# Optimization experiments

Measured on AMD Instinct MI355X. Metric: run time of the kernel, lower is better.

## Reference

```python
import jax, jax.numpy as jnp
import numpy as np

B, H, E, L = 2048, 4096, 8, 512
TAU = 1.0


def setup_inputs() -> dict:
    key = jax.random.key(0)
    k1, k2, k3, k4 = jax.random.split(key, 4)
    hidden = jax.random.normal(k1, (B, H), dtype=jnp.float32)
    envs = jax.random.normal(k2, (B, E), dtype=jnp.float32)
    idx = jnp.arange(B, dtype=jnp.int64)
    gumbel = jax.random.gumbel(k3, (B, E), dtype=jnp.float32)
    W = jax.random.normal(k4, (E, L, H), dtype=jnp.float32) * (1.0 / np.sqrt(H))
    return {"hidden": hidden, "envs": envs, "idx": idx, "gumbel": gumbel, "W": W}


def _hard_gumbel_softmax(log_probs, gumbel, tau):
    # F.gumbel_softmax(log_probs, tau=1, hard=True) with pre-sampled gumbel noise
    y_soft = jax.nn.softmax((log_probs + gumbel) / tau, axis=-1)
    y_hard = jax.nn.one_hot(jnp.argmax(y_soft, axis=-1), y_soft.shape[-1], dtype=y_soft.dtype)
    # straight-through estimator
    return y_hard + y_soft - jax.lax.stop_gradient(y_soft)


def reference(hidden, envs, idx, gumbel, W):
    # gating: env = gumbel_softmax(log_softmax(envs[idx]))  -> [B, E]
    log_probs = jax.nn.log_softmax(envs[idx], axis=-1)
    env = _hard_gumbel_softmax(log_probs, gumbel, TAU)
    # per-expert logits: [B, E, L]; fuses the per-sample python loop
    expert_logits = jnp.einsum("bh,elh->bel", hidden, W)
    # gating combine: [B, L]
    logits = jnp.einsum("be,bel->bl", env, expert_logits)
    # variance penalty over expert weights
    W_mean = jnp.mean(W, axis=0)  # [L, H]
    diff_sq = jnp.sum((W - W_mean[None]) ** 2, axis=(1, 2))  # ||W_e - W_mean||_2^2 per expert
    l1 = jnp.sum(jnp.abs(W), axis=(1, 2))                    # ||W_e||_1 per expert
    loss_penalty = jnp.mean(diff_sq / (l1 ** 2))
    return logits, loss_penalty
```

## Files before the change

### kernel.cpp

```cpp
#include <hip/hip_runtime.h>
#include <hip/hip_bf16.h>

constexpr int B = 2048, H = 4096, E = 8, L = 512;
constexpr int LH = L * H;

typedef float f4v __attribute__((ext_vector_type(4)));
typedef short short8 __attribute__((ext_vector_type(8)));

constexpr int BT = 128;
constexpr int LT = 128;
constexpr int KT = 32;
constexpr int SK = 4;
constexpr int RTMAX = 3;
constexpr int NITER = (H / SK) / KT;

constexpr int NGEMM = E * 4 * 4 * RTMAX;
constexpr int NPEN = 2048;

constexpr size_t WS_COUNTS = 0;
constexpr size_t WS_ACCUM = 32;
constexpr size_t WS_ROWLIST = 128;

using as1_u32 = const __attribute__((address_space(1))) unsigned int;
using as3_u32 = __attribute__((address_space(3))) unsigned int;

static __device__ __forceinline__ void dma16(const float* g, float* lds) {
  __builtin_amdgcn_global_load_lds((as1_u32*)g, (as3_u32*)lds, 16, 0, 0);
}

static __device__ __forceinline__ unsigned pk2(float a, float b) {
  __hip_bfloat162 p = __float22bfloat162_rn(make_float2(a, b));
  unsigned u;
  __builtin_memcpy(&u, &p, 4);
  return u;
}

static __device__ __forceinline__ short8 cvt8(f4v lo, f4v hi) {
  union { short8 s; unsigned u[4]; } r;
  r.u[0] = pk2(lo.x, lo.y);
  r.u[1] = pk2(lo.z, lo.w);
  r.u[2] = pk2(hi.x, hi.y);
  r.u[3] = pk2(hi.z, hi.w);
  return r.s;
}

__global__ void prep_kernel(const float* __restrict__ envs,
                            const float* __restrict__ gumbel,
                            int* __restrict__ counts,
                            float* __restrict__ accum,
                            int* __restrict__ row_list,
                            float* __restrict__ out) {
  const int t = threadIdx.x;
  const int id = blockIdx.x;
  if (id < E) {
    __shared__ int lcnt;
    if (t == 0) lcnt = 0;
    if (id == 0) {
      if (t < 16) accum[t] = 0.f;
    }
    __syncthreads();
#pragma unroll
    for (int r = 0; r < 8; ++r) {
      int b = r * 256 + t;
      f4v e0 = *(const f4v*)(envs + b * E);
      f4v e1 = *(const f4v*)(envs + b * E + 4);
      f4v g0 = *(const f4v*)(gumbel + b * E);
      f4v g1 = *(const f4v*)(gumbel + b * E + 4);
      float z[8] = {e0.x + g0.x, e0.y + g0.y, e0.z + g0.z, e0.w + g0.w,
                    e1.x + g1.x, e1.y + g1.y, e1.z + g1.z, e1.w + g1.w};
      float zmax = z[0];
      int am = 0;
#pragma unroll
      for (int e = 1; e < E; ++e)
        if (z[e] > zmax) { zmax = z[e]; am = e; }
      if (am == id) {
        int pos = atomicAdd(&lcnt, 1);
        row_list[id * B + pos] = b;
      }
    }
    __syncthreads();
    if (t == 0) counts[id] = lcnt;
  } else {
    const int cb = id - E;
    f4v z = {0.f, 0.f, 0.f, 0.f};
    f4v* dst = (f4v*)out + (size_t)cb * 1024;
#pragma unroll
    for (int i = 0; i < 4; ++i) dst[i * 256 + t] = z;
  }
}

__launch_bounds__(256, 2)
__global__ void fused_kernel(const float* __restrict__ hidden,
                             const float* __restrict__ W,
                             const int* __restrict__ counts,
                             const int* __restrict__ row_list,
                             float* __restrict__ out,
                             float* __restrict__ accum) {
  const int id = blockIdx.x;
  const int t = threadIdx.x;

  __shared__ __align__(16) float AshF[2][BT * KT];
  __shared__ __align__(16) float BshF[2][LT * KT];
  __shared__ int rlsh[BT];
  __shared__ float red[4][16];

  if (id >= NGEMM) {
    const int p = (id - NGEMM) * 256 + t;

    f4v w[E];
    float mx = 0.f, my = 0.f, mz = 0.f, mw = 0.f;
#pragma unroll
    for (int e = 0; e < E; ++e) {
      w[e] = __builtin_nontemporal_load(
          (const f4v*)(W + (size_t)e * LH + (size_t)p * 4));
      mx += w[e].x; my += w[e].y; mz += w[e].z; mw += w[e].w;
    }
    mx *= 0.125f; my *= 0.125f; mz *= 0.125f; mw *= 0.125f;

    float vals[16];
#pragma unroll
    for (int e = 0; e < E; ++e) {
      float dx = w[e].x - mx, dy = w[e].y - my, dz = w[e].z - mz,
            dw = w[e].w - mw;
      vals[e] = dx * dx + dy * dy + dz * dz + dw * dw;
      vals[8 + e] =
          fabsf(w[e].x) + fabsf(w[e].y) + fabsf(w[e].z) + fabsf(w[e].w);
    }
#pragma unroll
    for (int k = 0; k < 16; ++k) {
      float v = vals[k];
      for (int off = 32; off > 0; off >>= 1) v += __shfl_xor(v, off);
      vals[k] = v;
    }
    const int wv = t >> 6, lane = t & 63;
    if (lane == 0) {
#pragma unroll
      for (int k = 0; k < 16; ++k) red[wv][k] = vals[k];
    }
    __syncthreads();
    if (t < 16) {
      atomicAdd(&accum[t], red[0][t] + red[1][t] + red[2][t] + red[3][t]);
    }
    return;
  }

  const int e = id & 7;
  const int lt = (id >> 3) & 3;
  const int sk = (id >> 5) & 3;
  const int rt = id >> 7;

  const int cnt = counts[e];
  const int rbase = rt * BT;
  if (rbase >= cnt) return;
  const int lbase = lt * LT;

  if (t < BT) {
    int rr = rbase + t;
    rlsh[t] = row_list[e * B + (rr < cnt ? rr : (cnt - 1))];
  }
  __syncthreads();

  const float* Wp = W + (size_t)e * LH + (size_t)lbase * H;

  const int wave = t >> 6;
  const int lane = t & 63;
  const int quad = lane >> 4;
  const int l16 = lane & 15;
  const int wm = (wave >> 1) * 64;
  const int wn = (wave & 1) * 64;

  const int kbeg = sk * (H / SK);
  const int srow = lane >> 3;
  const int sblk = lane & 7;

  const float* sp[8];
  float* sl[2][8];
  const bool stageA = (wave < 2);
#pragma unroll
  for (int i = 0; i < 8; ++i) {
    int r = (stageA ? wave : (wave - 2)) * 64 + i * 8 + srow;
    int gblk = sblk ^ (r & 7);
    if (stageA) {
      sp[i] = hidden + (size_t)rlsh[r] * H + kbeg + gblk * 4;
      sl[0][i] = &AshF[0][(r - srow) * KT];
      sl[1][i] = &AshF[1][(r - srow) * KT];
    } else {
      sp[i] = Wp + (size_t)r * H + kbeg + gblk * 4;
      sl[0][i] = &BshF[0][(r - srow) * KT];
      sl[1][i] = &BshF[1][(r - srow) * KT];
    }
  }

  auto stage = [&](int buf) {
#pragma unroll
    for (int i = 0; i < 8; ++i) {
      dma16(sp[i], sl[buf][i]);
      sp[i] += KT;
    }
  };

  const int r7 = l16 & 7;
  const int slo = (2 * quad) ^ r7;
  const int shi = slo ^ 1;

  f4v acc[4][4] = {};

  stage(0);

  for (int it = 0; it < NITER; ++it) {
    const int buf = it & 1;
    __syncthreads();
    if (it + 1 < NITER) stage(buf ^ 1);

    short8 af[4], bf[4];
#pragma unroll
    for (int i = 0; i < 4; ++i) {
      int ra = wm + i * 16 + l16;
      f4v lo = *(const f4v*)&AshF[buf][ra * KT + slo * 4];
      f4v hi = *(const f4v*)&AshF[buf][ra * KT + shi * 4];
      af[i] = cvt8(lo, hi);
    }
#pragma unroll
    for (int j = 0; j < 4; ++j) {
      int rb = wn + j * 16 + l16;
      f4v lo = *(const f4v*)&BshF[buf][rb * KT + slo * 4];
      f4v hi = *(const f4v*)&BshF[buf][rb * KT + shi * 4];
      bf[j] = cvt8(lo, hi);
    }
#pragma unroll
    for (int i = 0; i < 4; ++i)
#pragma unroll
      for (int j = 0; j < 4; ++j)
        acc[i][j] =
            __builtin_amdgcn_mfma_f32_16x16x32_bf16(af[i], bf[j], acc[i][j],
                                                    0, 0, 0);
  }

#pragma unroll
  for (int i = 0; i < 4; ++i) {
#pragma unroll
    for (int j = 0; j < 4; ++j) {
#pragma unroll
      for (int reg = 0; reg < 4; ++reg) {
        int rloc = wm + i * 16 + quad * 4 + reg;
        if (rbase + rloc < cnt) {
          int bidx = rlsh[rloc];
          atomicAdd(&out[(size_t)bidx * L + lbase + wn + j * 16 + l16],
                    acc[i][j][reg]);
        }
      }
    }
  }
}

__global__ void finalize_kernel(const float* __restrict__ accum,
                                float* __restrict__ out) {
  if (threadIdx.x == 0) {
    float loss = 0.f;
#pragma unroll
    for (int e = 0; e < E; ++e) {
      float l1 = accum[8 + e];
      loss += accum[e] / (l1 * l1);
    }
    out[(size_t)B * L] = loss * 0.125f;
  }
}

extern "C" void kernel_launch(void* const* d_in, const int* in_sizes, int n_in,
                              void* d_out, int out_size, void* d_ws,
                              size_t ws_size, hipStream_t stream) {
  (void)in_sizes; (void)n_in; (void)ws_size; (void)out_size;
  const float* hidden = (const float*)d_in[0];
  const float* envs   = (const float*)d_in[1];
  const float* gumbel = (const float*)d_in[3];
  const float* W      = (const float*)d_in[4];
  float* out = (float*)d_out;

  char* ws = (char*)d_ws;
  int*   counts   = (int*)(ws + WS_COUNTS);
  float* accum    = (float*)(ws + WS_ACCUM);
  int*   row_list = (int*)(ws + WS_ROWLIST);

  prep_kernel<<<dim3(E + 256), dim3(256), 0, stream>>>(envs, gumbel, counts,
                                                       accum, row_list, out);
  fused_kernel<<<dim3(NGEMM + NPEN), dim3(256), 0, stream>>>(
      hidden, W, counts, row_list, out, accum);
  finalize_kernel<<<dim3(1), dim3(64), 0, stream>>>(accum, out);
}
```

Measured before the change: 173.2 us.

## Convert tiles to bf16 in registers before LDS and fold finalize into penalty blocks

```diff
diff --git a/kernel.cpp b/kernel.cpp
--- a/kernel.cpp
+++ b/kernel.cpp
@@ -10,6 +10,7 @@
 constexpr int BT = 128;
 constexpr int LT = 128;
 constexpr int KT = 32;
+constexpr int LROW = KT + 8;
 constexpr int SK = 4;
 constexpr int RTMAX = 3;
 constexpr int NITER = (H / SK) / KT;
@@ -19,14 +20,8 @@
 
 constexpr size_t WS_COUNTS = 0;
 constexpr size_t WS_ACCUM = 32;
+constexpr size_t WS_DONE = 96;
 constexpr size_t WS_ROWLIST = 128;
-
-using as1_u32 = const __attribute__((address_space(1))) unsigned int;
-using as3_u32 = __attribute__((address_space(3))) unsigned int;
-
-static __device__ __forceinline__ void dma16(const float* g, float* lds) {
-  __builtin_amdgcn_global_load_lds((as1_u32*)g, (as3_u32*)lds, 16, 0, 0);
-}
 
 static __device__ __forceinline__ unsigned pk2(float a, float b) {
   __hip_bfloat162 p = __float22bfloat162_rn(make_float2(a, b));
@@ -35,19 +30,24 @@
   return u;
 }
 
-static __device__ __forceinline__ short8 cvt8(f4v lo, f4v hi) {
-  union { short8 s; unsigned u[4]; } r;
-  r.u[0] = pk2(lo.x, lo.y);
-  r.u[1] = pk2(lo.z, lo.w);
-  r.u[2] = pk2(hi.x, hi.y);
-  r.u[3] = pk2(hi.z, hi.w);
-  return r.s;
+static __device__ __forceinline__ uint2 cvt4(f4v v) {
+  uint2 r;
+  r.x = pk2(v.x, v.y);
+  r.y = pk2(v.z, v.w);
+  return r;
+}
+
+static __device__ __forceinline__ void tbar() {
+  asm volatile("s_waitcnt lgkmcnt(0)" ::: "memory");
+  __builtin_amdgcn_s_barrier();
+  asm volatile("" ::: "memory");
 }
 
 __global__ void prep_kernel(const float* __restrict__ envs,
                             const float* __restrict__ gumbel,
                             int* __restrict__ counts,
                             float* __restrict__ accum,
+                            int* __restrict__ done,
                             int* __restrict__ row_list,
                             float* __restrict__ out) {
   const int t = threadIdx.x;
@@ -57,6 +57,7 @@
     if (t == 0) lcnt = 0;
     if (id == 0) {
       if (t < 16) accum[t] = 0.f;
+      if (t == 16) *done = 0;
     }
     __syncthreads();
 #pragma unroll
@@ -89,18 +90,19 @@
   }
 }
 
-__launch_bounds__(256, 2)
+__launch_bounds__(256, 3)
 __global__ void fused_kernel(const float* __restrict__ hidden,
                              const float* __restrict__ W,
                              const int* __restrict__ counts,
                              const int* __restrict__ row_list,
                              float* __restrict__ out,
-                             float* __restrict__ accum) {
+                             float* __restrict__ accum,
+                             int* __restrict__ done) {
   const int id = blockIdx.x;
   const int t = threadIdx.x;
 
-  __shared__ __align__(16) float AshF[2][BT * KT];
-  __shared__ __align__(16) float BshF[2][LT * KT];
+  __shared__ __align__(16) short Ash[2][BT * LROW];
+  __shared__ __align__(16) short Bsh[2][LT * LROW];
   __shared__ int rlsh[BT];
   __shared__ float red[4][16];
 
@@ -141,6 +143,21 @@
     if (t < 16) {
       atomicAdd(&accum[t], red[0][t] + red[1][t] + red[2][t] + red[3][t]);
     }
+    asm volatile("s_waitcnt vmcnt(0)" ::: "memory");
+    if (t == 0) {
+      int prev = __hip_atomic_fetch_add(done, 1, __ATOMIC_RELAXED,
+                                        __HIP_MEMORY_SCOPE_AGENT);
+      if (prev == NPEN - 1) {
+        float loss = 0.f;
+#pragma unroll
+        for (int e = 0; e < E; ++e) {
+          float d = atomicAdd(&accum[e], 0.f);
+          float l1 = atomicAdd(&accum[8 + e], 0.f);
+          loss += d / (l1 * l1);
+        }
+        out[(size_t)B * L] = loss * 0.125f;
+      }
+    }
     return;
   }
 
@@ -174,59 +191,55 @@
   const int sblk = lane & 7;
 
   const float* sp[8];
-  float* sl[2][8];
+  short* sw[8];
   const bool stageA = (wave < 2);
 #pragma unroll
   for (int i = 0; i < 8; ++i) {
     int r = (stageA ? wave : (wave - 2)) * 64 + i * 8 + srow;
-    int gblk = sblk ^ (r & 7);
     if (stageA) {
-      sp[i] = hidden + (size_t)rlsh[r] * H + kbeg + gblk * 4;
-      sl[0][i] = &AshF[0][(r - srow) * KT];
-      sl[1][i] = &AshF[1][(r - srow) * KT];
+      sp[i] = hidden + (size_t)rlsh[r] * H + kbeg + sblk * 4;
+      sw[i] = &Ash[0][r * LROW + sblk * 4];
     } else {
-      sp[i] = Wp + (size_t)r * H + kbeg + gblk * 4;
-      sl[0][i] = &BshF[0][(r - srow) * KT];
-      sl[1][i] = &BshF[1][(r - srow) * KT];
-    }
-  }
-
-  auto stage = [&](int buf) {
+      sp[i] = Wp + (size_t)r * H + kbeg + sblk * 4;
+      sw[i] = &Bsh[0][r * LROW + sblk * 4];
+    }
+  }
+
+  f4v g[8];
+  auto load8 = [&]() {
 #pragma unroll
     for (int i = 0; i < 8; ++i) {
-      dma16(sp[i], sl[buf][i]);
+      g[i] = *(const f4v*)sp[i];
       sp[i] += KT;
     }
   };
-
-  const int r7 = l16 & 7;
-  const int slo = (2 * quad) ^ r7;
-  const int shi = slo ^ 1;
+  auto write8 = [&](int buf) {
+#pragma unroll
+    for (int i = 0; i < 8; ++i) {
+      uint2 p = cvt4(g[i]);
+      *(uint2*)(sw[i] + buf * (BT * LROW)) = p;
+    }
+  };
 
   f4v acc[4][4] = {};
 
-  stage(0);
+  load8();
 
   for (int it = 0; it < NITER; ++it) {
     const int buf = it & 1;
-    __syncthreads();
-    if (it + 1 < NITER) stage(buf ^ 1);
-
+    write8(buf);
+    tbar();
+    if (it + 1 < NITER) load8();
+
+    const short* As = &Ash[0][0] + buf * (BT * LROW);
+    const short* Bs = &Bsh[0][0] + buf * (BT * LROW);
     short8 af[4], bf[4];
 #pragma unroll
-    for (int i = 0; i < 4; ++i) {
-      int ra = wm + i * 16 + l16;
-      f4v lo = *(const f4v*)&AshF[buf][ra * KT + slo * 4];
-      f4v hi = *(const f4v*)&AshF[buf][ra * KT + shi * 4];
-      af[i] = cvt8(lo, hi);
-    }
-#pragma unroll
-    for (int j = 0; j < 4; ++j) {
-      int rb = wn + j * 16 + l16;
-      f4v lo = *(const f4v*)&BshF[buf][rb * KT + slo * 4];
-      f4v hi = *(const f4v*)&BshF[buf][rb * KT + shi * 4];
-      bf[j] = cvt8(lo, hi);
-    }
+    for (int i = 0; i < 4; ++i)
+      af[i] = *(const short8*)&As[(wm + i * 16 + l16) * LROW + quad * 8];
+#pragma unroll
+    for (int j = 0; j < 4; ++j)
+      bf[j] = *(const short8*)&Bs[(wn + j * 16 + l16) * LROW + quad * 8];
 #pragma unroll
     for (int i = 0; i < 4; ++i)
 #pragma unroll
@@ -250,19 +263,6 @@
         }
       }
     }
-  }
-}
-
-__global__ void finalize_kernel(const float* __restrict__ accum,
-                                float* __restrict__ out) {
-  if (threadIdx.x == 0) {
-    float loss = 0.f;
-#pragma unroll
-    for (int e = 0; e < E; ++e) {
-      float l1 = accum[8 + e];
-      loss += accum[e] / (l1 * l1);
-    }
-    out[(size_t)B * L] = loss * 0.125f;
   }
 }
 
@@ -279,11 +279,12 @@
   char* ws = (char*)d_ws;
   int*   counts   = (int*)(ws + WS_COUNTS);
   float* accum    = (float*)(ws + WS_ACCUM);
+  int*   done     = (int*)(ws + WS_DONE);
   int*   row_list = (int*)(ws + WS_ROWLIST);
 
   prep_kernel<<<dim3(E + 256), dim3(256), 0, stream>>>(envs, gumbel, counts,
-                                                       accum, row_list, out);
+                                                       accum, done, row_list,
+                                                       out);
   fused_kernel<<<dim3(NGEMM + NPEN), dim3(256), 0, stream>>>(
-      hidden, W, counts, row_list, out, accum);
-  finalize_kernel<<<dim3(1), dim3(64), 0, stream>>>(accum, out);
-}
+      hidden, W, counts, row_list, out, accum, done);
+}
```

After: 188.7 us. 9.0% more time.

## Pre-convert W and hidden to bf16 in prep kernel and run GEMM on bf16

Applied to the files above, without the earlier changes.

```diff
diff --git a/kernel.cpp b/kernel.cpp
--- a/kernel.cpp
+++ b/kernel.cpp
@@ -16,15 +16,19 @@
 
 constexpr int NGEMM = E * 4 * 4 * RTMAX;
 constexpr int NPEN = 2048;
+constexpr int NHCV = 2048;
 
 constexpr size_t WS_COUNTS = 0;
 constexpr size_t WS_ACCUM = 32;
 constexpr size_t WS_ROWLIST = 128;
+constexpr size_t WS_W16 = 131072;
+constexpr size_t WS_A16 = WS_W16 + (size_t)E * LH * 2;
+constexpr size_t WS_NEED = WS_A16 + (size_t)B * H * 2;
 
 using as1_u32 = const __attribute__((address_space(1))) unsigned int;
 using as3_u32 = __attribute__((address_space(3))) unsigned int;
 
-static __device__ __forceinline__ void dma16(const float* g, float* lds) {
+static __device__ __forceinline__ void dma16(const void* g, void* lds) {
   __builtin_amdgcn_global_load_lds((as1_u32*)g, (as3_u32*)lds, 16, 0, 0);
 }
 
@@ -44,11 +48,22 @@
   return r.s;
 }
 
-__global__ void prep_kernel(const float* __restrict__ envs,
+static __device__ __forceinline__ uint2 cvt4(f4v v) {
+  uint2 r;
+  r.x = pk2(v.x, v.y);
+  r.y = pk2(v.z, v.w);
+  return r;
+}
+
+__global__ void prep_kernel(const float* __restrict__ hidden,
+                            const float* __restrict__ W,
+                            const float* __restrict__ envs,
                             const float* __restrict__ gumbel,
                             int* __restrict__ counts,
                             float* __restrict__ accum,
                             int* __restrict__ row_list,
+                            short* __restrict__ W16,
+                            short* __restrict__ A16,
                             float* __restrict__ out) {
   const int t = threadIdx.x;
   const int id = blockIdx.x;
@@ -80,17 +95,207 @@
     }
     __syncthreads();
     if (t == 0) counts[id] = lcnt;
-  } else {
+    return;
+  }
+  if (id < E + 256) {
     const int cb = id - E;
     f4v z = {0.f, 0.f, 0.f, 0.f};
     f4v* dst = (f4v*)out + (size_t)cb * 1024;
 #pragma unroll
     for (int i = 0; i < 4; ++i) dst[i * 256 + t] = z;
+    return;
+  }
+  if (id < E + 256 + NPEN) {
+    __shared__ float red[4][16];
+    const int p = (id - E - 256) * 256 + t;
+
+    f4v w[E];
+    float mx = 0.f, my = 0.f, mz = 0.f, mw = 0.f;
+#pragma unroll
+    for (int e = 0; e < E; ++e) {
+      w[e] = __builtin_nontemporal_load(
+          (const f4v*)(W + (size_t)e * LH + (size_t)p * 4));
+      mx += w[e].x; my += w[e].y; mz += w[e].z; mw += w[e].w;
+    }
+#pragma unroll
+    for (int e = 0; e < E; ++e) {
+      *(uint2*)(W16 + (size_t)e * LH + (size_t)p * 4) = cvt4(w[e]);
+    }
+    mx *= 0.125f; my *= 0.125f; mz *= 0.125f; mw *= 0.125f;
+
+    float vals[16];
+#pragma unroll
+    for (int e = 0; e < E; ++e) {
+      float dx = w[e].x - mx, dy = w[e].y - my, dz = w[e].z - mz,
+            dw = w[e].w - mw;
+      vals[e] = dx * dx + dy * dy + dz * dz + dw * dw;
+      vals[8 + e] =
+          fabsf(w[e].x) + fabsf(w[e].y) + fabsf(w[e].z) + fabsf(w[e].w);
+    }
+#pragma unroll
+    for (int k = 0; k < 16; ++k) {
+      float v = vals[k];
+      for (int off = 32; off > 0; off >>= 1) v += __shfl_xor(v, off);
+      vals[k] = v;
+    }
+    const int wv = t >> 6, lane = t & 63;
+    if (lane == 0) {
+#pragma unroll
+      for (int k = 0; k < 16; ++k) red[wv][k] = vals[k];
+    }
+    __syncthreads();
+    if (t < 16) {
+      atomicAdd(&accum[t], red[0][t] + red[1][t] + red[2][t] + red[3][t]);
+    }
+    return;
+  }
+  {
+    const int cb = id - E - 256 - NPEN;
+    const size_t base = ((size_t)cb * 256 + t) * 16;
+    f4v v0 = __builtin_nontemporal_load((const f4v*)(hidden + base));
+    f4v v1 = __builtin_nontemporal_load((const f4v*)(hidden + base + 4));
+    f4v v2 = __builtin_nontemporal_load((const f4v*)(hidden + base + 8));
+    f4v v3 = __builtin_nontemporal_load((const f4v*)(hidden + base + 12));
+    *(uint2*)(A16 + base) = cvt4(v0);
+    *(uint2*)(A16 + base + 4) = cvt4(v1);
+    *(uint2*)(A16 + base + 8) = cvt4(v2);
+    *(uint2*)(A16 + base + 12) = cvt4(v3);
   }
 }
 
 __launch_bounds__(256, 2)
-__global__ void fused_kernel(const float* __restrict__ hidden,
+__global__ void fused_bf16(const short* __restrict__ A16,
+                           const short* __restrict__ W16,
+                           const int* __restrict__ counts,
+                           const int* __restrict__ row_list,
+                           const float* __restrict__ accum,
+                           float* __restrict__ out) {
+  const int id = blockIdx.x;
+  const int t = threadIdx.x;
+
+  if (id >= NGEMM) {
+    if (t == 0) {
+      float loss = 0.f;
+#pragma unroll
+      for (int e = 0; e < E; ++e) {
+        float l1 = accum[8 + e];
+        loss += accum[e] / (l1 * l1);
+      }
+      out[(size_t)B * L] = loss * 0.125f;
+    }
+    return;
+  }
+
+  __shared__ __align__(16) short Ash[2][BT * KT];
+  __shared__ __align__(16) short Bsh[2][LT * KT];
+  __shared__ int rlsh[BT];
+
+  const int e = id & 7;
+  const int lt = (id >> 3) & 3;
+  const int sk = (id >> 5) & 3;
+  const int rt = id >> 7;
+
+  const int cnt = counts[e];
+  const int rbase = rt * BT;
+  if (rbase >= cnt) return;
+  const int lbase = lt * LT;
+
+  if (t < BT) {
+    int rr = rbase + t;
+    rlsh[t] = row_list[e * B + (rr < cnt ? rr : (cnt - 1))];
+  }
+  __syncthreads();
+
+  const short* Wp = W16 + (size_t)e * LH + (size_t)lbase * H;
+
+  const int wave = t >> 6;
+  const int lane = t & 63;
+  const int quad = lane >> 4;
+  const int l16 = lane & 15;
+  const int wm = (wave >> 1) * 64;
+  const int wn = (wave & 1) * 64;
+
+  const int kbeg = sk * (H / SK);
+  const int srow = lane >> 2;
+  const int sblk = lane & 3;
+
+  const short* sp[4];
+  short* sl[2][4];
+  const bool stageA = (wave < 2);
+#pragma unroll
+  for (int i = 0; i < 4; ++i) {
+    int r = (stageA ? wave : (wave - 2)) * 64 + i * 16 + srow;
+    int gblk = sblk ^ ((r >> 1) & 3);
+    if (stageA) {
+      sp[i] = A16 + (size_t)rlsh[r] * H + kbeg + gblk * 8;
+      sl[0][i] = &Ash[0][(r - srow) * KT];
+      sl[1][i] = &Ash[1][(r - srow) * KT];
+    } else {
+      sp[i] = Wp + (size_t)r * H + kbeg + gblk * 8;
+      sl[0][i] = &Bsh[0][(r - srow) * KT];
+      sl[1][i] = &Bsh[1][(r - srow) * KT];
+    }
+  }
+
+  auto stage = [&](int buf) {
+#pragma unroll
+    for (int i = 0; i < 4; ++i) {
+      dma16(sp[i], sl[buf][i]);
+      sp[i] += KT;
+    }
+  };
+
+  int aoff[4], boff[4];
+#pragma unroll
+  for (int i = 0; i < 4; ++i) {
+    int ra = wm + i * 16 + l16;
+    aoff[i] = ra * KT + (quad ^ ((ra >> 1) & 3)) * 8;
+    int rb = wn + i * 16 + l16;
+    boff[i] = rb * KT + (quad ^ ((rb >> 1) & 3)) * 8;
+  }
+
+  f4v acc[4][4] = {};
+
+  stage(0);
+
+  for (int it = 0; it < NITER; ++it) {
+    const int buf = it & 1;
+    __syncthreads();
+    if (it + 1 < NITER) stage(buf ^ 1);
+
+    short8 af[4], bf[4];
+#pragma unroll
+    for (int i = 0; i < 4; ++i) af[i] = *(const short8*)&Ash[buf][aoff[i]];
+#pragma unroll
+    for (int j = 0; j < 4; ++j) bf[j] = *(const short8*)&Bsh[buf][boff[j]];
+#pragma unroll
+    for (int i = 0; i < 4; ++i)
+#pragma unroll
+      for (int j = 0; j < 4; ++j)
+        acc[i][j] =
+            __builtin_amdgcn_mfma_f32_16x16x32_bf16(af[i], bf[j], acc[i][j],
+                                                    0, 0, 0);
+  }
+
+#pragma unroll
+  for (int i = 0; i < 4; ++i) {
+#pragma unroll
+    for (int j = 0; j < 4; ++j) {
+#pragma unroll
+      for (int reg = 0; reg < 4; ++reg) {
+        int rloc = wm + i * 16 + quad * 4 + reg;
+        if (rbase + rloc < cnt) {
+          int bidx = rlsh[rloc];
+          atomicAdd(&out[(size_t)bidx * L + lbase + wn + j * 16 + l16],
+                    acc[i][j][reg]);
+        }
+      }
+    }
+  }
+}
+
+__launch_bounds__(256, 2)
+__global__ void fused_legacy(const float* __restrict__ hidden,
                              const float* __restrict__ W,
                              const int* __restrict__ counts,
                              const int* __restrict__ row_list,
@@ -106,7 +311,6 @@
 
   if (id >= NGEMM) {
     const int p = (id - NGEMM) * 256 + t;
-
     f4v w[E];
     float mx = 0.f, my = 0.f, mz = 0.f, mw = 0.f;
 #pragma unroll
@@ -116,7 +320,6 @@
       mx += w[e].x; my += w[e].y; mz += w[e].z; mw += w[e].w;
     }
     mx *= 0.125f; my *= 0.125f; mz *= 0.125f; mw *= 0.125f;
-
     float vals[16];
 #pragma unroll
     for (int e = 0; e < E; ++e) {
@@ -161,14 +364,12 @@
   __syncthreads();
 
   const float* Wp = W + (size_t)e * LH + (size_t)lbase * H;
-
   const int wave = t >> 6;
   const int lane = t & 63;
   const int quad = lane >> 4;
   const int l16 = lane & 15;
   const int wm = (wave >> 1) * 64;
   const int wn = (wave & 1) * 64;
-
   const int kbeg = sk * (H / SK);
   const int srow = lane >> 3;
   const int sblk = lane & 7;
@@ -190,7 +391,6 @@
       sl[1][i] = &BshF[1][(r - srow) * KT];
     }
   }
-
   auto stage = [&](int buf) {
 #pragma unroll
     for (int i = 0; i < 8; ++i) {
@@ -204,14 +404,11 @@
   const int shi = slo ^ 1;
 
   f4v acc[4][4] = {};
-
   stage(0);
-
   for (int it = 0; it < NITER; ++it) {
     const int buf = it & 1;
     __syncthreads();
     if (it + 1 < NITER) stage(buf ^ 1);
-
     short8 af[4], bf[4];
 #pragma unroll
     for (int i = 0; i < 4; ++i) {
@@ -235,7 +432,6 @@
             __builtin_amdgcn_mfma_f32_16x16x32_bf16(af[i], bf[j], acc[i][j],
                                                     0, 0, 0);
   }
-
 #pragma unroll
   for (int i = 0; i < 4; ++i) {
 #pragma unroll
@@ -269,7 +465,7 @@
 extern "C" void kernel_launch(void* const* d_in, const int* in_sizes, int n_in,
                               void* d_out, int out_size, void* d_ws,
                               size_t ws_size, hipStream_t stream) {
-  (void)in_sizes; (void)n_in; (void)ws_size; (void)out_size;
+  (void)in_sizes; (void)n_in; (void)out_size;
   const float* hidden = (const float*)d_in[0];
   const float* envs   = (const float*)d_in[1];
   const float* gumbel = (const float*)d_in[3];
@@ -280,10 +476,19 @@
   int*   counts   = (int*)(ws + WS_COUNTS);
   float* accum    = (float*)(ws + WS_ACCUM);
   int*   row_list = (int*)(ws + WS_ROWLIST);
-
-  prep_kernel<<<dim3(E + 256), dim3(256), 0, stream>>>(envs, gumbel, counts,
-                                                       accum, row_list, out);
-  fused_kernel<<<dim3(NGEMM + NPEN), dim3(256), 0, stream>>>(
-      hidden, W, counts, row_list, out, accum);
-  finalize_kernel<<<dim3(1), dim3(64), 0, stream>>>(accum, out);
-}
+  short* W16      = (short*)(ws + WS_W16);
+  short* A16      = (short*)(ws + WS_A16);
+
+  if (ws_size >= WS_NEED) {
+    prep_kernel<<<dim3(E + 256 + NPEN + NHCV), dim3(256), 0, stream>>>(
+        hidden, W, envs, gumbel, counts, accum, row_list, W16, A16, out);
+    fused_bf16<<<dim3(NGEMM + 1), dim3(256), 0, stream>>>(
+        A16, W16, counts, row_list, accum, out);
+  } else {
+    prep_kernel<<<dim3(E + 256), dim3(256), 0, stream>>>(
+        hidden, W, envs, gumbel, counts, accum, row_list, W16, A16, out);
+    fused_legacy<<<dim3(NGEMM + NPEN), dim3(256), 0, stream>>>(
+        hidden, W, counts, row_list, out, accum);
+    finalize_kernel<<<dim3(1), dim3(64), 0, stream>>>(accum, out);
+  }
+}
```

Result: slower. 183.8 us (+6.2%).

## Pre-convert hidden to bf16 in prep kernel and stage bf16 A tiles

Applied to the files above, without the earlier changes.

```diff
diff --git a/kernel.cpp b/kernel.cpp
--- a/kernel.cpp
+++ b/kernel.cpp
@@ -16,15 +16,18 @@
 
 constexpr int NGEMM = E * 4 * 4 * RTMAX;
 constexpr int NPEN = 2048;
+constexpr int NCONV = 2048;
 
 constexpr size_t WS_COUNTS = 0;
 constexpr size_t WS_ACCUM = 32;
 constexpr size_t WS_ROWLIST = 128;
+constexpr size_t WS_A16 = 131072;
+constexpr size_t WS_NEED = WS_A16 + (size_t)B * H * 2;
 
 using as1_u32 = const __attribute__((address_space(1))) unsigned int;
 using as3_u32 = __attribute__((address_space(3))) unsigned int;
 
-static __device__ __forceinline__ void dma16(const float* g, float* lds) {
+static __device__ __forceinline__ void dma16(const void* g, void* lds) {
   __builtin_amdgcn_global_load_lds((as1_u32*)g, (as3_u32*)lds, 16, 0, 0);
 }
 
@@ -44,11 +47,20 @@
   return r.s;
 }
 
-__global__ void prep_kernel(const float* __restrict__ envs,
+static __device__ __forceinline__ uint2 cvt4(f4v v) {
+  uint2 r;
+  r.x = pk2(v.x, v.y);
+  r.y = pk2(v.z, v.w);
+  return r;
+}
+
+__global__ void prep_kernel(const float* __restrict__ hidden,
+                            const float* __restrict__ envs,
                             const float* __restrict__ gumbel,
                             int* __restrict__ counts,
                             float* __restrict__ accum,
                             int* __restrict__ row_list,
+                            short* __restrict__ A16,
                             float* __restrict__ out) {
   const int t = threadIdx.x;
   const int id = blockIdx.x;
@@ -80,17 +92,32 @@
     }
     __syncthreads();
     if (t == 0) counts[id] = lcnt;
-  } else {
+    return;
+  }
+  if (id < E + 256) {
     const int cb = id - E;
     f4v z = {0.f, 0.f, 0.f, 0.f};
     f4v* dst = (f4v*)out + (size_t)cb * 1024;
 #pragma unroll
     for (int i = 0; i < 4; ++i) dst[i * 256 + t] = z;
-  }
-}
-
-__launch_bounds__(256, 2)
-__global__ void fused_kernel(const float* __restrict__ hidden,
+    return;
+  }
+  {
+    const int cb = id - E - 256;
+    const size_t base = ((size_t)cb * 256 + t) * 16;
+    f4v v0 = __builtin_nontemporal_load((const f4v*)(hidden + base));
+    f4v v1 = __builtin_nontemporal_load((const f4v*)(hidden + base + 4));
+    f4v v2 = __builtin_nontemporal_load((const f4v*)(hidden + base + 8));
+    f4v v3 = __builtin_nontemporal_load((const f4v*)(hidden + base + 12));
+    *(uint2*)(A16 + base) = cvt4(v0);
+    *(uint2*)(A16 + base + 4) = cvt4(v1);
+    *(uint2*)(A16 + base + 8) = cvt4(v2);
+    *(uint2*)(A16 + base + 12) = cvt4(v3);
+  }
+}
+
+__launch_bounds__(256, 3)
+__global__ void fused_kernel(const short* __restrict__ A16,
                              const float* __restrict__ W,
                              const int* __restrict__ counts,
                              const int* __restrict__ row_list,
@@ -99,7 +126,7 @@
   const int id = blockIdx.x;
   const int t = threadIdx.x;
 
-  __shared__ __align__(16) float AshF[2][BT * KT];
+  __shared__ __align__(16) short Ash[2][BT * KT];
   __shared__ __align__(16) float BshF[2][LT * KT];
   __shared__ int rlsh[BT];
   __shared__ float red[4][16];
@@ -170,35 +197,59 @@
   const int wn = (wave & 1) * 64;
 
   const int kbeg = sk * (H / SK);
-  const int srow = lane >> 3;
-  const int sblk = lane & 7;
-
-  const float* sp[8];
-  float* sl[2][8];
   const bool stageA = (wave < 2);
-#pragma unroll
-  for (int i = 0; i < 8; ++i) {
-    int r = (stageA ? wave : (wave - 2)) * 64 + i * 8 + srow;
-    int gblk = sblk ^ (r & 7);
+
+  const int srowA = lane >> 2;
+  const int sblkA = lane & 3;
+  const short* spa[4];
+  short* sla[2][4];
+  const int srowB = lane >> 3;
+  const int sblkB = lane & 7;
+  const float* spb[8];
+  float* slb[2][8];
+
+  if (stageA) {
+#pragma unroll
+    for (int i = 0; i < 4; ++i) {
+      int r = wave * 64 + i * 16 + srowA;
+      int gblk = sblkA ^ ((r >> 1) & 3);
+      spa[i] = A16 + (size_t)rlsh[r] * H + kbeg + gblk * 8;
+      sla[0][i] = &Ash[0][(r - srowA) * KT];
+      sla[1][i] = &Ash[1][(r - srowA) * KT];
+    }
+  } else {
+#pragma unroll
+    for (int i = 0; i < 8; ++i) {
+      int r = (wave - 2) * 64 + i * 8 + srowB;
+      int gblk = sblkB ^ (r & 7);
+      spb[i] = Wp + (size_t)r * H + kbeg + gblk * 4;
+      slb[0][i] = &BshF[0][(r - srowB) * KT];
+      slb[1][i] = &BshF[1][(r - srowB) * KT];
+    }
+  }
+
+  auto stage = [&](int buf) {
     if (stageA) {
-      sp[i] = hidden + (size_t)rlsh[r] * H + kbeg + gblk * 4;
-      sl[0][i] = &AshF[0][(r - srow) * KT];
-      sl[1][i] = &AshF[1][(r - srow) * KT];
+#pragma unroll
+      for (int i = 0; i < 4; ++i) {
+        dma16(spa[i], sla[buf][i]);
+        spa[i] += KT;
+      }
     } else {
-      sp[i] = Wp + (size_t)r * H + kbeg + gblk * 4;
-      sl[0][i] = &BshF[0][(r - srow) * KT];
-      sl[1][i] = &BshF[1][(r - srow) * KT];
-    }
-  }
-
-  auto stage = [&](int buf) {
-#pragma unroll
-    for (int i = 0; i < 8; ++i) {
-      dma16(sp[i], sl[buf][i]);
-      sp[i] += KT;
+#pragma unroll
+      for (int i = 0; i < 8; ++i) {
+        dma16(spb[i], slb[buf][i]);
+        spb[i] += KT;
+      }
     }
   };
 
+  int aoff[4];
+#pragma unroll
+  for (int i = 0; i < 4; ++i) {
+    int ra = wm + i * 16 + l16;
+    aoff[i] = ra * KT + (quad ^ ((ra >> 1) & 3)) * 8;
+  }
   const int r7 = l16 & 7;
   const int slo = (2 * quad) ^ r7;
   const int shi = slo ^ 1;
@@ -214,12 +265,7 @@
 
     short8 af[4], bf[4];
 #pragma unroll
-    for (int i = 0; i < 4; ++i) {
-      int ra = wm + i * 16 + l16;
-      f4v lo = *(const f4v*)&AshF[buf][ra * KT + slo * 4];
-      f4v hi = *(const f4v*)&AshF[buf][ra * KT + shi * 4];
-      af[i] = cvt8(lo, hi);
-    }
+    for (int i = 0; i < 4; ++i) af[i] = *(const short8*)&Ash[buf][aoff[i]];
 #pragma unroll
     for (int j = 0; j < 4; ++j) {
       int rb = wn + j * 16 + l16;
@@ -269,7 +315,7 @@
 extern "C" void kernel_launch(void* const* d_in, const int* in_sizes, int n_in,
                               void* d_out, int out_size, void* d_ws,
                               size_t ws_size, hipStream_t stream) {
-  (void)in_sizes; (void)n_in; (void)ws_size; (void)out_size;
+  (void)in_sizes; (void)n_in; (void)out_size; (void)ws_size;
   const float* hidden = (const float*)d_in[0];
   const float* envs   = (const float*)d_in[1];
   const float* gumbel = (const float*)d_in[3];
@@ -280,10 +326,11 @@
   int*   counts   = (int*)(ws + WS_COUNTS);
   float* accum    = (float*)(ws + WS_ACCUM);
   int*   row_list = (int*)(ws + WS_ROWLIST);
-
-  prep_kernel<<<dim3(E + 256), dim3(256), 0, stream>>>(envs, gumbel, counts,
-                                                       accum, row_list, out);
+  short* A16      = (short*)(ws + WS_A16);
+
+  prep_kernel<<<dim3(E + 256 + NCONV), dim3(256), 0, stream>>>(
+      hidden, envs, gumbel, counts, accum, row_list, A16, out);
   fused_kernel<<<dim3(NGEMM + NPEN), dim3(256), 0, stream>>>(
-      hidden, W, counts, row_list, out, accum);
+      A16, W, counts, row_list, out, accum);
   finalize_kernel<<<dim3(1), dim3(64), 0, stream>>>(accum, out);
 }
```

After: 184.2 us. 1.06x slower.
